# Optimization experiments

Measured on AMD Instinct MI355X. Metric: run time of the kernel, lower is better.

The kernel has to match this reference:

```python
import jax, jax.numpy as jnp
import numpy as np

B, N, D = 4, 512, 256  # batch, num_diseases, feature_dim == hidden_dim
H = 256                # hidden_dim
EPS = 1e-5

def _layernorm(x, g, b):
    m = jnp.mean(x, axis=-1, keepdims=True)
    v = jnp.mean((x - m) ** 2, axis=-1, keepdims=True)
    return (x - m) * jax.lax.rsqrt(v + EPS) * g + b

def setup_inputs() -> dict:
    key = jax.random.key(0)
    ks = jax.random.split(key, 16)
    s = 0.02
    return {
        "x": jax.random.normal(ks[0], (B, N, D), jnp.float32),
        "area_matrix": jax.random.uniform(ks[1], (B, N), jnp.float32),
        "co_occurrence": jax.random.uniform(ks[2], (N, N), jnp.float32),
        "Wq": jax.random.normal(ks[3], (H, D), jnp.float32) * s,
        "bq": jnp.zeros((H,), jnp.float32),
        "Wk": jax.random.normal(ks[4], (H, D), jnp.float32) * s,
        "bk": jnp.zeros((H,), jnp.float32),
        "Wv": jax.random.normal(ks[5], (H, D), jnp.float32) * s,
        "bv": jnp.zeros((H,), jnp.float32),
        "We1": jax.random.normal(ks[6], (H, 2), jnp.float32) * 0.5,
        "be1": jnp.zeros((H,), jnp.float32),
        "We2": jax.random.normal(ks[7], (1, H), jnp.float32) * s,
        "be2": jnp.zeros((1,), jnp.float32),
        "Wo": jax.random.normal(ks[8], (H, H), jnp.float32) * s,
        "bo": jnp.zeros((H,), jnp.float32),
        "g_ot": jnp.ones((H,), jnp.float32),
        "b_ot": jnp.zeros((H,), jnp.float32),
        "g1": jnp.ones((H,), jnp.float32),
        "b1": jnp.zeros((H,), jnp.float32),
        "g2": jnp.ones((H,), jnp.float32),
        "b2": jnp.zeros((H,), jnp.float32),
    }

def reference(x, area_matrix, co_occurrence, Wq, bq, Wk, bk, Wv, bv,
              We1, be1, We2, be2, Wo, bo, g_ot, b_ot, g1, b1, g2, b2):
    # projections: (B, N, H)
    q = jnp.einsum('bnd,hd->bnh', x, Wq) + bq
    k = jnp.einsum('bnd,hd->bnh', x, Wk) + bk
    v = jnp.einsum('bnd,hd->bnh', x, Wv) + bv
    attn_scores = jnp.einsum('bih,bjh->bij', q, k) / jnp.sqrt(jnp.float32(H))
    # edge inputs: (B, N, N, 2) = stack(broadcast area along last N, broadcast co-occ along batch)
    area = jnp.broadcast_to(area_matrix[:, :, None], (B, N, N))
    co = jnp.broadcast_to(co_occurrence[None], (B, N, N))
    edge_inputs = jnp.stack([area, co], axis=-1)
    h = jax.nn.relu(jnp.einsum('bije,he->bijh', edge_inputs, We1) + be1)
    edge_weights = jax.nn.sigmoid(jnp.einsum('bijh,oh->bijo', h, We2) + be2)[..., 0]
    attn_probs = jax.nn.softmax(attn_scores * edge_weights, axis=-1)  # dropout = identity (eval)
    out = jnp.einsum('bij,bjh->bih', attn_probs, v)
    out = _layernorm(out, g1, b1)
    out = jax.nn.relu(_layernorm(jnp.einsum('bnh,oh->bno', out, Wo) + bo, g_ot, b_ot))
    out = _layernorm(out + x, g2, b2)
    return out
```

## Files before the change

### kernel.cpp

```cpp
#include <hip/hip_runtime.h>

typedef unsigned short u16;
typedef unsigned int u32;

#define NB 4
#define NN 512
#define ND 256
#define NH 256
#define TI 4

typedef __attribute__((ext_vector_type(8))) short short8;
typedef __attribute__((ext_vector_type(4))) float f32x4;

__device__ __forceinline__ u16 f2bf(float f) {
    u32 t; __builtin_memcpy(&t, &f, 4);
    u32 r = (t + 0x7FFFu + ((t >> 16) & 1u)) >> 16;
    return (u16)r;
}

__device__ __forceinline__ float4 blockReduce4(float4 v, float4* red4b, bool ismax) {
#pragma unroll
    for (int o = 32; o > 0; o >>= 1) {
        float4 t;
        t.x = __shfl_down(v.x, o); t.y = __shfl_down(v.y, o);
        t.z = __shfl_down(v.z, o); t.w = __shfl_down(v.w, o);
        if (ismax) {
            v.x = fmaxf(v.x, t.x); v.y = fmaxf(v.y, t.y);
            v.z = fmaxf(v.z, t.z); v.w = fmaxf(v.w, t.w);
        } else {
            v.x += t.x; v.y += t.y; v.z += t.z; v.w += t.w;
        }
    }
    int wid = threadIdx.x >> 6;
    __syncthreads();
    if ((threadIdx.x & 63) == 0) red4b[wid] = v;
    __syncthreads();
    float4 r = red4b[0];
#pragma unroll
    for (int w = 1; w < 8; ++w) {
        float4 u = red4b[w];
        if (ismax) {
            r.x = fmaxf(r.x, u.x); r.y = fmaxf(r.y, u.y);
            r.z = fmaxf(r.z, u.z); r.w = fmaxf(r.w, u.w);
        } else {
            r.x += u.x; r.y += u.y; r.z += u.z; r.w += u.w;
        }
    }
    return r;
}

__global__ __launch_bounds__(256) void convert_k(
    const float* __restrict__ x, const float* __restrict__ Wq,
    const float* __restrict__ Wk, const float* __restrict__ Wv,
    u16* __restrict__ xb, u16* __restrict__ Wb)
{
    int t = blockIdx.x * 256 + threadIdx.x;
    if (t < 524288) {
        xb[t] = f2bf(x[t]);
    } else {
        int u = t - 524288;
        const float* src = (u < 65536) ? Wq : (u < 131072) ? Wk : Wv;
        Wb[u] = f2bf(src[u & 65535]);
    }
}

__global__ __launch_bounds__(256) void transpose_wo(
    const float* __restrict__ Wo, float* __restrict__ Wot)
{
    __shared__ float t[32][33];
    const int tx = threadIdx.x & 31, ty = threadIdx.x >> 5;
#pragma unroll
    for (int k = 0; k < 4; ++k)
        t[ty + 8 * k][tx] = Wo[(blockIdx.y * 32 + ty + 8 * k) * 256 + blockIdx.x * 32 + tx];
    __syncthreads();
#pragma unroll
    for (int k = 0; k < 4; ++k)
        Wot[(blockIdx.x * 32 + ty + 8 * k) * 256 + blockIdx.y * 32 + tx] = t[tx][ty + 8 * k];
}

__global__ __launch_bounds__(256) void qkv_mfma(
    const u16* __restrict__ xb, const u16* __restrict__ Wb,
    const float* __restrict__ bq, const float* __restrict__ bk, const float* __restrict__ bv,
    float* __restrict__ q, float* __restrict__ k_t, float* __restrict__ v)
{
    const int lane = threadIdx.x & 63, wave = threadIdx.x >> 6;
    const int r0 = blockIdx.x * 64 + wave * 16;
    const int out0 = blockIdx.y * 16;
    const int which = blockIdx.y >> 4;
    const float* bia = (which == 0) ? bq : (which == 1) ? bk : bv;

    const int m = lane & 15, koff = (lane >> 4) * 8;
    const u16* Ap = xb + (size_t)(r0 + m) * 256 + koff;
    const u16* Bp = Wb + (size_t)(out0 + m) * 256 + koff;

    f32x4 acc = {0.f, 0.f, 0.f, 0.f};
#pragma unroll
    for (int kb = 0; kb < 8; ++kb) {
        short8 a  = *(const short8*)(Ap + kb * 32);
        short8 bf = *(const short8*)(Bp + kb * 32);
        acc = __builtin_amdgcn_mfma_f32_16x16x32_bf16(a, bf, acc, 0, 0, 0);
    }

    const int oc = (out0 + m) & 255;
    const float bias = bia[oc];
    const int rbase = r0 + (lane >> 4) * 4;
#pragma unroll
    for (int reg = 0; reg < 4; ++reg) {
        int R = rbase + reg;
        float val = acc[reg] + bias;
        if (which == 1)      k_t[((size_t)(R >> 9) * 256 + oc) * 512 + (R & 511)] = val;
        else if (which == 0) q[(size_t)R * 256 + oc] = val;
        else                 v[(size_t)R * 256 + oc] = val;
    }
}

__global__ __launch_bounds__(512) void fused_kernel(
    const float* __restrict__ x, const float* __restrict__ area, const float* __restrict__ co,
    const float* __restrict__ We1, const float* __restrict__ be1,
    const float* __restrict__ We2, const float* __restrict__ be2,
    const float* __restrict__ Wot, const float* __restrict__ bo,
    const float* __restrict__ g_ot, const float* __restrict__ b_ot,
    const float* __restrict__ g1, const float* __restrict__ b1,
    const float* __restrict__ g2, const float* __restrict__ b2,
    const float* __restrict__ q, const float* __restrict__ k_t, const float* __restrict__ v,
    float* __restrict__ out)
{
    const int tid = threadIdx.x;
    const int b = blockIdx.x >> 7;
    const int i0 = (blockIdx.x & 127) << 2;

    __shared__ float ts[TI * 256];
    __shared__ float ea[TI * 256];
    __shared__ float eb[TI * 256];
    __shared__ float srow[TI * 512];
    __shared__ float4 red4b[8];

    const float be2f = be2[0];

    float4 bS4 = make_float4(0, 0, 0, 0), bB4 = make_float4(0, 0, 0, 0);
    if (tid < 256) {
        const float w10 = We1[2 * tid], w11 = We1[2 * tid + 1];
        const float w2v = We2[tid], be1v = be1[tid];
#pragma unroll
        for (int ti = 0; ti < TI; ++ti) {
            const float a = area[b * NN + i0 + ti];
            float al = fmaf(a, w10, be1v);
            float s = w11 * w2v, bb = al * w2v;
            float t = 3e38f, es = 0.f, ebv = 0.f, baS = 0.f, baB = 0.f;
            if (w11 == 0.f) {
                if (al > 0.f) baB = bb;
            } else {
                float tt = -al / w11;
                if (w11 > 0.f) {
                    if (tt <= 0.f)      { baS = s; baB = bb; }
                    else if (tt < 1.f)  { t = tt; es = s; ebv = bb; }
                } else {
                    if (tt >= 1.f)      { baS = s; baB = bb; }
                    else if (tt > 0.f)  { t = tt; es = -s; ebv = -bb; baS = s; baB = bb; }
                }
            }
            ts[ti * 256 + tid] = t; ea[ti * 256 + tid] = es; eb[ti * 256 + tid] = ebv;
            ((float*)&bS4)[ti] = baS; ((float*)&bB4)[ti] = baB;
        }
    }
    const float4 baseS4 = blockReduce4(bS4, red4b, false);
    const float4 baseB4 = blockReduce4(bB4, red4b, false);

    {
        const int tiS = tid >> 7, pidS = tid & 127;
        for (int k2 = 2; k2 <= 256; k2 <<= 1) {
            for (int jj = k2 >> 1; jj > 0; jj >>= 1) {
                __syncthreads();
                int low = pidS & (jj - 1);
                int t = ((pidS - low) << 1) + low;
                int p = t + jj;
                bool up = ((t & k2) == 0);
                int a0 = tiS * 256 + t, a1 = tiS * 256 + p;
                float t0 = ts[a0], t1 = ts[a1];
                if ((t0 > t1) == up) {
                    ts[a0] = t1; ts[a1] = t0;
                    float u = ea[a0]; ea[a0] = ea[a1]; ea[a1] = u;
                    u = eb[a0]; eb[a0] = eb[a1]; eb[a1] = u;
                }
            }
        }
        __syncthreads();
    }

    {
        const int colS = tid & 255, tiA = (tid >> 8) * 2;
        for (int off = 1; off < 256; off <<= 1) {
            float va0 = ea[tiA * 256 + colS],       vb0 = eb[tiA * 256 + colS];
            float va1 = ea[(tiA + 1) * 256 + colS], vb1 = eb[(tiA + 1) * 256 + colS];
            if (colS >= off) {
                va0 += ea[tiA * 256 + colS - off];       vb0 += eb[tiA * 256 + colS - off];
                va1 += ea[(tiA + 1) * 256 + colS - off]; vb1 += eb[(tiA + 1) * 256 + colS - off];
            }
            __syncthreads();
            ea[tiA * 256 + colS] = va0;       eb[tiA * 256 + colS] = vb0;
            ea[(tiA + 1) * 256 + colS] = va1; eb[(tiA + 1) * 256 + colS] = vb1;
            __syncthreads();
        }
    }

    float sA[TI];
    {
        const int j = tid;
        float dot[TI] = {0.f, 0.f, 0.f, 0.f};
        const float* kt = k_t + (size_t)b * NH * NN;
        const float* qb_ = q + (size_t)(b * NN + i0) * NH;
        for (int h = 0; h < 256; h += 4) {
            float k0 = kt[(size_t)(h + 0) * 512 + j];
            float k1 = kt[(size_t)(h + 1) * 512 + j];
            float k2c = kt[(size_t)(h + 2) * 512 + j];
            float k3 = kt[(size_t)(h + 3) * 512 + j];
#pragma unroll
            for (int ti = 0; ti < TI; ++ti) {
                float4 qv = *(const float4*)&qb_[ti * 256 + h];
                dot[ti] += qv.x * k0 + qv.y * k1 + qv.z * k2c + qv.w * k3;
            }
        }
#pragma unroll
        for (int ti = 0; ti < TI; ++ti) {
            float c = co[(size_t)(i0 + ti) * NN + j];
            int r = 0;
#pragma unroll
            for (int st = 128; st; st >>= 1)
                if (ts[ti * 256 + r + st - 1] <= c) r += st;
            float S = ((const float*)&baseS4)[ti] + (r ? ea[ti * 256 + r - 1] : 0.f);
            float B = ((const float*)&baseB4)[ti] + (r ? eb[ti * 256 + r - 1] : 0.f);
            float e = fmaf(c, S, B);
            float ew = 1.f / (1.f + __expf(-(e + be2f)));
            sA[ti] = dot[ti] * 0.0625f * ew;
        }
    }

    {
        float4 m4 = make_float4(sA[0], sA[1], sA[2], sA[3]);
        m4 = blockReduce4(m4, red4b, true);
        float eA[TI];
        float4 sum4;
#pragma unroll
        for (int ti = 0; ti < TI; ++ti) {
            eA[ti] = __expf(sA[ti] - ((const float*)&m4)[ti]);
            ((float*)&sum4)[ti] = eA[ti];
        }
        sum4 = blockReduce4(sum4, red4b, false);
#pragma unroll
        for (int ti = 0; ti < TI; ++ti)
            srow[ti * 512 + tid] = eA[ti] / ((const float*)&sum4)[ti];
        __syncthreads();
    }

    const int hP = tid & 255, half = tid >> 8;
    float accv[TI] = {0.f, 0.f, 0.f, 0.f};
    {
        const float* vp = v + (size_t)b * NN * NH + hP;
        for (int j4 = half * 64; j4 < half * 64 + 64; ++j4) {
            const int jj = 4 * j4;
            float v0 = vp[(size_t)(jj + 0) * NH];
            float v1 = vp[(size_t)(jj + 1) * NH];
            float v2 = vp[(size_t)(jj + 2) * NH];
            float v3 = vp[(size_t)(jj + 3) * NH];
#pragma unroll
            for (int ti = 0; ti < TI; ++ti) {
                float4 p4 = *(const float4*)&srow[ti * 512 + jj];
                accv[ti] += p4.x * v0 + p4.y * v1 + p4.z * v2 + p4.w * v3;
            }
        }
    }
    __syncthreads();
    if (half == 1) {
#pragma unroll
        for (int ti = 0; ti < TI; ++ti) ts[ti * 256 + hP] = accv[ti];
    }
    __syncthreads();
    if (half == 0) {
#pragma unroll
        for (int ti = 0; ti < TI; ++ti) accv[ti] += ts[ti * 256 + hP];
    }

    float4 t4;
    float dd[TI];
#pragma unroll
    for (int ti = 0; ti < TI; ++ti) ((float*)&t4)[ti] = (half == 0) ? accv[ti] : 0.f;
    float4 mean4 = blockReduce4(t4, red4b, false);
#pragma unroll
    for (int ti = 0; ti < TI; ++ti) {
        dd[ti] = (half == 0) ? accv[ti] - ((const float*)&mean4)[ti] * (1.f / 256.f) : 0.f;
        ((float*)&t4)[ti] = dd[ti] * dd[ti];
    }
    float4 var4 = blockReduce4(t4, red4b, false);
    if (half == 0) {
        const float g1v = g1[hP], b1v = b1[hP];
#pragma unroll
        for (int ti = 0; ti < TI; ++ti)
            srow[ti * 256 + hP] = dd[ti] * rsqrtf(((const float*)&var4)[ti] * (1.f / 256.f) + 1e-5f) * g1v + b1v;
    }
    __syncthreads();

    float acc2[TI] = {0.f, 0.f, 0.f, 0.f};
    {
        for (int d4 = half * 32; d4 < half * 32 + 32; ++d4) {
            const int d = 4 * d4;
            float w0 = Wot[(size_t)(d + 0) * 256 + hP];
            float w1 = Wot[(size_t)(d + 1) * 256 + hP];
            float w2c = Wot[(size_t)(d + 2) * 256 + hP];
            float w3 = Wot[(size_t)(d + 3) * 256 + hP];
#pragma unroll
            for (int ti = 0; ti < TI; ++ti) {
                float4 y4 = *(const float4*)&srow[ti * 256 + d];
                acc2[ti] += y4.x * w0 + y4.y * w1 + y4.z * w2c + y4.w * w3;
            }
        }
    }
    __syncthreads();
    if (half == 1) {
#pragma unroll
        for (int ti = 0; ti < TI; ++ti) ts[ti * 256 + hP] = acc2[ti];
    }
    __syncthreads();
    if (half == 0) {
        const float bov = bo[hP];
#pragma unroll
        for (int ti = 0; ti < TI; ++ti) acc2[ti] += ts[ti * 256 + hP] + bov;
    }

#pragma unroll
    for (int ti = 0; ti < TI; ++ti) ((float*)&t4)[ti] = (half == 0) ? acc2[ti] : 0.f;
    mean4 = blockReduce4(t4, red4b, false);
#pragma unroll
    for (int ti = 0; ti < TI; ++ti) {
        dd[ti] = (half == 0) ? acc2[ti] - ((const float*)&mean4)[ti] * (1.f / 256.f) : 0.f;
        ((float*)&t4)[ti] = dd[ti] * dd[ti];
    }
    var4 = blockReduce4(t4, red4b, false);
    float z[TI];
    const float gotv = (half == 0) ? g_ot[hP] : 0.f;
    const float botv = (half == 0) ? b_ot[hP] : 0.f;
#pragma unroll
    for (int ti = 0; ti < TI; ++ti)
        z[ti] = fmaxf(dd[ti] * rsqrtf(((const float*)&var4)[ti] * (1.f / 256.f) + 1e-5f) * gotv + botv, 0.f);

    float tt[TI];
#pragma unroll
    for (int ti = 0; ti < TI; ++ti) {
        tt[ti] = (half == 0) ? z[ti] + x[(size_t)(b * NN + i0 + ti) * ND + hP] : 0.f;
        ((float*)&t4)[ti] = tt[ti];
    }
    mean4 = blockReduce4(t4, red4b, false);
#pragma unroll
    for (int ti = 0; ti < TI; ++ti) {
        dd[ti] = (half == 0) ? tt[ti] - ((const float*)&mean4)[ti] * (1.f / 256.f) : 0.f;
        ((float*)&t4)[ti] = dd[ti] * dd[ti];
    }
    var4 = blockReduce4(t4, red4b, false);
    if (half == 0) {
        const float g2v = g2[hP], b2v = b2[hP];
#pragma unroll
        for (int ti = 0; ti < TI; ++ti) {
            float o = dd[ti] * rsqrtf(((const float*)&var4)[ti] * (1.f / 256.f) + 1e-5f) * g2v + b2v;
            out[(size_t)(b * NN + i0 + ti) * NH + hP] = o;
        }
    }
}

extern "C" void kernel_launch(void* const* d_in, const int* in_sizes, int n_in,
                              void* d_out, int out_size, void* d_ws, size_t ws_size,
                              hipStream_t stream) {
    const float* x    = (const float*)d_in[0];
    const float* area = (const float*)d_in[1];
    const float* co   = (const float*)d_in[2];
    const float* Wq   = (const float*)d_in[3];
    const float* bq   = (const float*)d_in[4];
    const float* Wk   = (const float*)d_in[5];
    const float* bk   = (const float*)d_in[6];
    const float* Wv   = (const float*)d_in[7];
    const float* bv   = (const float*)d_in[8];
    const float* We1  = (const float*)d_in[9];
    const float* be1  = (const float*)d_in[10];
    const float* We2  = (const float*)d_in[11];
    const float* be2  = (const float*)d_in[12];
    const float* Wo   = (const float*)d_in[13];
    const float* bo   = (const float*)d_in[14];
    const float* g_ot = (const float*)d_in[15];
    const float* b_ot = (const float*)d_in[16];
    const float* g1   = (const float*)d_in[17];
    const float* b1   = (const float*)d_in[18];
    const float* g2   = (const float*)d_in[19];
    const float* b2   = (const float*)d_in[20];

    float* q   = (float*)d_ws;
    float* k_t = q + (size_t)NB * NN * NH;
    float* v   = k_t + (size_t)NB * NN * NH;
    float* Wot = v + (size_t)NB * NN * NH;
    u16*   xb  = (u16*)(Wot + 256 * 256);
    u16*   Wb  = xb + (size_t)NB * NN * ND;

    convert_k<<<2816, 256, 0, stream>>>(x, Wq, Wk, Wv, xb, Wb);
    transpose_wo<<<dim3(8, 8), 256, 0, stream>>>(Wo, Wot);
    qkv_mfma<<<dim3(32, 48), 256, 0, stream>>>(xb, Wb, bq, bk, bv, q, k_t, v);
    fused_kernel<<<NB * NN / TI, 512, 0, stream>>>(x, area, co, We1, be1, We2, be2, Wot, bo,
                                                   g_ot, b_ot, g1, b1, g2, b2, q, k_t, v,
                                                   (float*)d_out);
}
```

Before: 175.6 us.

## Fuse bf16 conversion and Wo transpose into QKV kernel; histogram edge weights

Drops the separate convert and transpose launches. The QKV MFMA kernel now reads fp32 inputs and converts them to bf16 in registers, and an extra grid row does the Wo transpose. In the fused kernel, the per-row bitonic sort plus binary search over edge breakpoints is replaced by a 256-bin shared-memory histogram built with atomics and a ping-pong prefix scan. This removes many barriers but quantizes the piecewise-linear edge MLP to bins, which can change results when a breakpoint and a co-occurrence value land in the same bin.

```diff
diff --git a/kernel.cpp b/kernel.cpp
--- a/kernel.cpp
+++ b/kernel.cpp
@@ -12,10 +12,16 @@
 typedef __attribute__((ext_vector_type(8))) short short8;
 typedef __attribute__((ext_vector_type(4))) float f32x4;
 
-__device__ __forceinline__ u16 f2bf(float f) {
+__device__ __forceinline__ short bf(float f) {
     u32 t; __builtin_memcpy(&t, &f, 4);
     u32 r = (t + 0x7FFFu + ((t >> 16) & 1u)) >> 16;
-    return (u16)r;
+    return (short)(u16)r;
+}
+
+__device__ __forceinline__ float waveReduceSum(float v) {
+#pragma unroll
+    for (int o = 32; o > 0; o >>= 1) v += __shfl_down(v, o);
+    return v;
 }
 
 __device__ __forceinline__ float4 blockReduce4(float4 v, float4* red4b, bool ismax) {
@@ -49,56 +55,59 @@
     return r;
 }
 
-__global__ __launch_bounds__(256) void convert_k(
-    const float* __restrict__ x, const float* __restrict__ Wq,
-    const float* __restrict__ Wk, const float* __restrict__ Wv,
-    u16* __restrict__ xb, u16* __restrict__ Wb)
+__global__ __launch_bounds__(256) void qkv_mfma(
+    const float* __restrict__ x,
+    const float* __restrict__ Wq, const float* __restrict__ bq,
+    const float* __restrict__ Wk, const float* __restrict__ bk,
+    const float* __restrict__ Wv, const float* __restrict__ bv,
+    const float* __restrict__ Wo,
+    float* __restrict__ q, float* __restrict__ k_t, float* __restrict__ v,
+    float* __restrict__ Wot)
 {
-    int t = blockIdx.x * 256 + threadIdx.x;
-    if (t < 524288) {
-        xb[t] = f2bf(x[t]);
-    } else {
-        int u = t - 524288;
-        const float* src = (u < 65536) ? Wq : (u < 131072) ? Wk : Wv;
-        Wb[u] = f2bf(src[u & 65535]);
-    }
-}
-
-__global__ __launch_bounds__(256) void transpose_wo(
-    const float* __restrict__ Wo, float* __restrict__ Wot)
-{
-    __shared__ float t[32][33];
-    const int tx = threadIdx.x & 31, ty = threadIdx.x >> 5;
-#pragma unroll
-    for (int k = 0; k < 4; ++k)
-        t[ty + 8 * k][tx] = Wo[(blockIdx.y * 32 + ty + 8 * k) * 256 + blockIdx.x * 32 + tx];
-    __syncthreads();
-#pragma unroll
-    for (int k = 0; k < 4; ++k)
-        Wot[(blockIdx.x * 32 + ty + 8 * k) * 256 + blockIdx.y * 32 + tx] = t[tx][ty + 8 * k];
-}
-
-__global__ __launch_bounds__(256) void qkv_mfma(
-    const u16* __restrict__ xb, const u16* __restrict__ Wb,
-    const float* __restrict__ bq, const float* __restrict__ bk, const float* __restrict__ bv,
-    float* __restrict__ q, float* __restrict__ k_t, float* __restrict__ v)
-{
-    const int lane = threadIdx.x & 63, wave = threadIdx.x >> 6;
+    const int tid = threadIdx.x;
+    if (blockIdx.y == 48) {
+        __shared__ float t[32][33];
+        const int tx = tid & 31, ty = tid >> 5;
+#pragma unroll
+        for (int tt2 = 0; tt2 < 2; ++tt2) {
+            const int tile = blockIdx.x * 2 + tt2;
+            const int bx = tile & 7, by = tile >> 3;
+            __syncthreads();
+#pragma unroll
+            for (int k = 0; k < 4; ++k)
+                t[ty + 8 * k][tx] = Wo[(size_t)(by * 32 + ty + 8 * k) * 256 + bx * 32 + tx];
+            __syncthreads();
+#pragma unroll
+            for (int k = 0; k < 4; ++k)
+                Wot[(size_t)(bx * 32 + ty + 8 * k) * 256 + by * 32 + tx] = t[tx][ty + 8 * k];
+        }
+        return;
+    }
+
+    const int lane = tid & 63, wave = tid >> 6;
     const int r0 = blockIdx.x * 64 + wave * 16;
     const int out0 = blockIdx.y * 16;
     const int which = blockIdx.y >> 4;
+    const float* W   = (which == 0) ? Wq : (which == 1) ? Wk : Wv;
     const float* bia = (which == 0) ? bq : (which == 1) ? bk : bv;
 
     const int m = lane & 15, koff = (lane >> 4) * 8;
-    const u16* Ap = xb + (size_t)(r0 + m) * 256 + koff;
-    const u16* Bp = Wb + (size_t)(out0 + m) * 256 + koff;
+    const float* Ap = x + (size_t)(r0 + m) * 256 + koff;
+    const float* Bp = W + (size_t)((out0 & 255) + m) * 256 + koff;
 
     f32x4 acc = {0.f, 0.f, 0.f, 0.f};
 #pragma unroll
     for (int kb = 0; kb < 8; ++kb) {
-        short8 a  = *(const short8*)(Ap + kb * 32);
-        short8 bf = *(const short8*)(Bp + kb * 32);
-        acc = __builtin_amdgcn_mfma_f32_16x16x32_bf16(a, bf, acc, 0, 0, 0);
+        float4 a0 = *(const float4*)(Ap + kb * 32);
+        float4 a1 = *(const float4*)(Ap + kb * 32 + 4);
+        float4 b0 = *(const float4*)(Bp + kb * 32);
+        float4 b1 = *(const float4*)(Bp + kb * 32 + 4);
+        short8 af, bf8;
+        af[0] = bf(a0.x); af[1] = bf(a0.y); af[2] = bf(a0.z); af[3] = bf(a0.w);
+        af[4] = bf(a1.x); af[5] = bf(a1.y); af[6] = bf(a1.z); af[7] = bf(a1.w);
+        bf8[0] = bf(b0.x); bf8[1] = bf(b0.y); bf8[2] = bf(b0.z); bf8[3] = bf(b0.w);
+        bf8[4] = bf(b1.x); bf8[5] = bf(b1.y); bf8[6] = bf(b1.z); bf8[7] = bf(b1.w);
+        acc = __builtin_amdgcn_mfma_f32_16x16x32_bf16(af, bf8, acc, 0, 0, 0);
     }
 
     const int oc = (out0 + m) & 255;
@@ -128,109 +137,102 @@
     const int tid = threadIdx.x;
     const int b = blockIdx.x >> 7;
     const int i0 = (blockIdx.x & 127) << 2;
-
-    __shared__ float ts[TI * 256];
-    __shared__ float ea[TI * 256];
-    __shared__ float eb[TI * 256];
-    __shared__ float srow[TI * 512];
+    const int lane = tid & 63, w = tid >> 6;
+
+    __shared__ float histS[1024], histB[1024], hist2S[1024], hist2B[1024];
+    __shared__ float srow[2048];
     __shared__ float4 red4b[8];
+    __shared__ float sBaseS[4], sBaseB[4], redA[8], redB[8];
 
     const float be2f = be2[0];
 
-    float4 bS4 = make_float4(0, 0, 0, 0), bB4 = make_float4(0, 0, 0, 0);
-    if (tid < 256) {
-        const float w10 = We1[2 * tid], w11 = We1[2 * tid + 1];
-        const float w2v = We2[tid], be1v = be1[tid];
-#pragma unroll
-        for (int ti = 0; ti < TI; ++ti) {
-            const float a = area[b * NN + i0 + ti];
-            float al = fmaf(a, w10, be1v);
-            float s = w11 * w2v, bb = al * w2v;
-            float t = 3e38f, es = 0.f, ebv = 0.f, baS = 0.f, baB = 0.f;
+    histS[tid] = 0.f; histS[tid + 512] = 0.f;
+    histB[tid] = 0.f; histB[tid + 512] = 0.f;
+    __syncthreads();
+    {
+        const int s = tid >> 7, h0 = tid & 127;
+        const float a = area[b * NN + i0 + s];
+        float baS = 0.f, baB = 0.f;
+#pragma unroll
+        for (int k = 0; k < 2; ++k) {
+            const int h = h0 + 128 * k;
+            const float w10 = We1[2 * h], w11 = We1[2 * h + 1];
+            const float w2v = We2[h], be1v = be1[h];
+            const float al = fmaf(a, w10, be1v);
+            const float sl = w11 * w2v, bb = al * w2v;
             if (w11 == 0.f) {
-                if (al > 0.f) baB = bb;
+                if (al > 0.f) baB += bb;
             } else {
                 float tt = -al / w11;
                 if (w11 > 0.f) {
-                    if (tt <= 0.f)      { baS = s; baB = bb; }
-                    else if (tt < 1.f)  { t = tt; es = s; ebv = bb; }
+                    if (tt <= 0.f)      { baS += sl; baB += bb; }
+                    else if (tt < 1.f) {
+                        int u = (int)(tt * 256.f); u = u > 255 ? 255 : u;
+                        atomicAdd(&histS[s * 256 + u], sl);
+                        atomicAdd(&histB[s * 256 + u], bb);
+                    }
                 } else {
-                    if (tt >= 1.f)      { baS = s; baB = bb; }
-                    else if (tt > 0.f)  { t = tt; es = -s; ebv = -bb; baS = s; baB = bb; }
+                    if (tt >= 1.f)      { baS += sl; baB += bb; }
+                    else if (tt > 0.f) {
+                        baS += sl; baB += bb;
+                        int u = (int)(tt * 256.f); u = u > 255 ? 255 : u;
+                        atomicAdd(&histS[s * 256 + u], -sl);
+                        atomicAdd(&histB[s * 256 + u], -bb);
+                    }
                 }
             }
-            ts[ti * 256 + tid] = t; ea[ti * 256 + tid] = es; eb[ti * 256 + tid] = ebv;
-            ((float*)&bS4)[ti] = baS; ((float*)&bB4)[ti] = baB;
-        }
-    }
-    const float4 baseS4 = blockReduce4(bS4, red4b, false);
-    const float4 baseB4 = blockReduce4(bB4, red4b, false);
-
-    {
-        const int tiS = tid >> 7, pidS = tid & 127;
-        for (int k2 = 2; k2 <= 256; k2 <<= 1) {
-            for (int jj = k2 >> 1; jj > 0; jj >>= 1) {
-                __syncthreads();
-                int low = pidS & (jj - 1);
-                int t = ((pidS - low) << 1) + low;
-                int p = t + jj;
-                bool up = ((t & k2) == 0);
-                int a0 = tiS * 256 + t, a1 = tiS * 256 + p;
-                float t0 = ts[a0], t1 = ts[a1];
-                if ((t0 > t1) == up) {
-                    ts[a0] = t1; ts[a1] = t0;
-                    float u = ea[a0]; ea[a0] = ea[a1]; ea[a1] = u;
-                    u = eb[a0]; eb[a0] = eb[a1]; eb[a1] = u;
-                }
+        }
+        float rS = waveReduceSum(baS), rB = waveReduceSum(baB);
+        if (lane == 0) { redA[w] = rS; redB[w] = rB; }
+    }
+    __syncthreads();
+    if (tid < 4) {
+        sBaseS[tid] = redA[2 * tid] + redA[2 * tid + 1];
+        sBaseB[tid] = redB[2 * tid] + redB[2 * tid + 1];
+    }
+
+    {
+        float* sa = histS; float* sb = histB; float* da = hist2S; float* db = hist2B;
+        const int col = tid & 255;
+        const int s2 = (tid >> 8) * 2;
+        for (int off = 1; off < 256; off <<= 1) {
+            const int i1 = s2 * 256 + col, i2 = (s2 + 1) * 256 + col;
+            float v1a = sa[i1], v1b = sb[i1], v2a = sa[i2], v2b = sb[i2];
+            if (col >= off) {
+                v1a += sa[i1 - off]; v1b += sb[i1 - off];
+                v2a += sa[i2 - off]; v2b += sb[i2 - off];
             }
-        }
-        __syncthreads();
-    }
-
-    {
-        const int colS = tid & 255, tiA = (tid >> 8) * 2;
-        for (int off = 1; off < 256; off <<= 1) {
-            float va0 = ea[tiA * 256 + colS],       vb0 = eb[tiA * 256 + colS];
-            float va1 = ea[(tiA + 1) * 256 + colS], vb1 = eb[(tiA + 1) * 256 + colS];
-            if (colS >= off) {
-                va0 += ea[tiA * 256 + colS - off];       vb0 += eb[tiA * 256 + colS - off];
-                va1 += ea[(tiA + 1) * 256 + colS - off]; vb1 += eb[(tiA + 1) * 256 + colS - off];
-            }
+            da[i1] = v1a; db[i1] = v1b; da[i2] = v2a; db[i2] = v2b;
             __syncthreads();
-            ea[tiA * 256 + colS] = va0;       eb[tiA * 256 + colS] = vb0;
-            ea[(tiA + 1) * 256 + colS] = va1; eb[(tiA + 1) * 256 + colS] = vb1;
-            __syncthreads();
+            float* t = sa; sa = da; da = t;
+            t = sb; sb = db; db = t;
         }
     }
 
     float sA[TI];
     {
-        const int j = tid;
+        const float* kt = k_t + (size_t)b * NH * NN + tid;
+        const float* qb_ = q + (size_t)(b * NN + i0) * NH;
         float dot[TI] = {0.f, 0.f, 0.f, 0.f};
-        const float* kt = k_t + (size_t)b * NH * NN;
-        const float* qb_ = q + (size_t)(b * NN + i0) * NH;
         for (int h = 0; h < 256; h += 4) {
-            float k0 = kt[(size_t)(h + 0) * 512 + j];
-            float k1 = kt[(size_t)(h + 1) * 512 + j];
-            float k2c = kt[(size_t)(h + 2) * 512 + j];
-            float k3 = kt[(size_t)(h + 3) * 512 + j];
+            float k0 = kt[(size_t)(h + 0) * 512];
+            float k1 = kt[(size_t)(h + 1) * 512];
+            float k2 = kt[(size_t)(h + 2) * 512];
+            float k3 = kt[(size_t)(h + 3) * 512];
 #pragma unroll
             for (int ti = 0; ti < TI; ++ti) {
                 float4 qv = *(const float4*)&qb_[ti * 256 + h];
-                dot[ti] += qv.x * k0 + qv.y * k1 + qv.z * k2c + qv.w * k3;
+                dot[ti] += qv.x * k0 + qv.y * k1 + qv.z * k2 + qv.w * k3;
             }
         }
 #pragma unroll
         for (int ti = 0; ti < TI; ++ti) {
-            float c = co[(size_t)(i0 + ti) * NN + j];
-            int r = 0;
-#pragma unroll
-            for (int st = 128; st; st >>= 1)
-                if (ts[ti * 256 + r + st - 1] <= c) r += st;
-            float S = ((const float*)&baseS4)[ti] + (r ? ea[ti * 256 + r - 1] : 0.f);
-            float B = ((const float*)&baseB4)[ti] + (r ? eb[ti * 256 + r - 1] : 0.f);
-            float e = fmaf(c, S, B);
-            float ew = 1.f / (1.f + __expf(-(e + be2f)));
+            float c = co[(size_t)(i0 + ti) * NN + tid];
+            int u = (int)(c * 256.f); u = u > 255 ? 255 : u;
+            float S = sBaseS[ti] + histS[ti * 256 + u];
+            float B = sBaseB[ti] + histB[ti * 256 + u];
+            float e = fmaf(c, S, B) + be2f;
+            float ew = 1.f / (1.f + __expf(-e));
             sA[ti] = dot[ti] * 0.0625f * ew;
         }
     }
@@ -239,16 +241,16 @@
         float4 m4 = make_float4(sA[0], sA[1], sA[2], sA[3]);
         m4 = blockReduce4(m4, red4b, true);
         float eA[TI];
-        float4 sum4;
+        float4 s4;
 #pragma unroll
         for (int ti = 0; ti < TI; ++ti) {
             eA[ti] = __expf(sA[ti] - ((const float*)&m4)[ti]);
-            ((float*)&sum4)[ti] = eA[ti];
-        }
-        sum4 = blockReduce4(sum4, red4b, false);
+            ((float*)&s4)[ti] = eA[ti];
+        }
+        s4 = blockReduce4(s4, red4b, false);
 #pragma unroll
         for (int ti = 0; ti < TI; ++ti)
-            srow[ti * 512 + tid] = eA[ti] / ((const float*)&sum4)[ti];
+            srow[ti * 512 + tid] = eA[ti] * (1.f / ((const float*)&s4)[ti]);
         __syncthreads();
     }
 
@@ -268,16 +270,15 @@
                 accv[ti] += p4.x * v0 + p4.y * v1 + p4.z * v2 + p4.w * v3;
             }
         }
-    }
-    __syncthreads();
-    if (half == 1) {
-#pragma unroll
-        for (int ti = 0; ti < TI; ++ti) ts[ti * 256 + hP] = accv[ti];
-    }
-    __syncthreads();
-    if (half == 0) {
-#pragma unroll
-        for (int ti = 0; ti < TI; ++ti) accv[ti] += ts[ti * 256 + hP];
+        if (half == 1) {
+#pragma unroll
+            for (int ti = 0; ti < TI; ++ti) hist2S[ti * 256 + hP] = accv[ti];
+        }
+        __syncthreads();
+        if (half == 0) {
+#pragma unroll
+            for (int ti = 0; ti < TI; ++ti) accv[ti] += hist2S[ti * 256 + hP];
+        }
     }
 
     float4 t4;
@@ -313,17 +314,16 @@
                 acc2[ti] += y4.x * w0 + y4.y * w1 + y4.z * w2c + y4.w * w3;
             }
         }
-    }
-    __syncthreads();
-    if (half == 1) {
-#pragma unroll
-        for (int ti = 0; ti < TI; ++ti) ts[ti * 256 + hP] = acc2[ti];
-    }
-    __syncthreads();
-    if (half == 0) {
-        const float bov = bo[hP];
-#pragma unroll
-        for (int ti = 0; ti < TI; ++ti) acc2[ti] += ts[ti * 256 + hP] + bov;
+        if (half == 1) {
+#pragma unroll
+            for (int ti = 0; ti < TI; ++ti) histS[ti * 256 + hP] = acc2[ti];
+        }
+        __syncthreads();
+        if (half == 0) {
+            const float bov = bo[hP];
+#pragma unroll
+            for (int ti = 0; ti < TI; ++ti) acc2[ti] += histS[ti * 256 + hP] + bov;
+        }
     }
 
 #pragma unroll
@@ -394,12 +394,9 @@
     float* k_t = q + (size_t)NB * NN * NH;
     float* v   = k_t + (size_t)NB * NN * NH;
     float* Wot = v + (size_t)NB * NN * NH;
-    u16*   xb  = (u16*)(Wot + 256 * 256);
-    u16*   Wb  = xb + (size_t)NB * NN * ND;
-
-    convert_k<<<2816, 256, 0, stream>>>(x, Wq, Wk, Wv, xb, Wb);
-    transpose_wo<<<dim3(8, 8), 256, 0, stream>>>(Wo, Wot);
-    qkv_mfma<<<dim3(32, 48), 256, 0, stream>>>(xb, Wb, bq, bk, bv, q, k_t, v);
+
+    qkv_mfma<<<dim3(32, 49), 256, 0, stream>>>(x, Wq, bq, Wk, bk, Wv, bv, Wo,
+                                               q, k_t, v, Wot);
     fused_kernel<<<NB * NN / TI, 512, 0, stream>>>(x, area, co, We1, be1, We2, be2, Wot, bo,
                                                    g_ot, b_ot, g1, b1, g2, b2, q, k_t, v,
                                                    (float*)d_out);
```

After: 172.0 us. 1.02x faster.
